# Optimization experiments

Hardware: AMD Instinct MI355X
Metric: run time of the kernel (lower is better)

The kernel has to match this reference:

```python
import jax, jax.numpy as jnp
import numpy as np

N = 8192

def _gcn_layer(x, src, dst, W, b, norm_out, norm_in, activation=None):
    # DGL GraphConv, norm='both': D_in^{-1/2} A D_out^{-1/2} X W + b
    xw = x @ W                              # [N, out] (weight first: in>=out)
    m = (xw * norm_out[:, None])[src]       # gather per-edge messages [E, out]
    agg = jax.ops.segment_sum(m, dst, num_segments=N)
    h = agg * norm_in[:, None] + b
    return activation(h) if activation is not None else h


def setup_inputs() -> dict:
    key = jax.random.key(0)
    k1, k2, k3, k4, k5 = jax.random.split(key, 5)
    E = 262144
    in_dim, h1, h2 = 512, 256, 64
    features = jax.random.normal(k1, (N, in_dim), dtype=jnp.float32)
    src = jax.random.randint(k2, (E,), 0, N)
    dst = jax.random.randint(k3, (E,), 0, N)
    W1 = jax.random.normal(k4, (in_dim, h1), dtype=jnp.float32) / np.sqrt(in_dim)
    b1 = jnp.zeros((h1,), dtype=jnp.float32)
    W2 = jax.random.normal(k5, (h1, h2), dtype=jnp.float32) / np.sqrt(h1)
    b2 = jnp.zeros((h2,), dtype=jnp.float32)
    return {"features": features, "src": src, "dst": dst,
            "W1": W1, "b1": b1, "W2": W2, "b2": b2}


def reference(features, src, dst, W1, b1, W2, b2):
    # Degrees and symmetric normalization (clamp(min=1) as in DGL GraphConv).
    ones = jnp.ones(src.shape[0], dtype=features.dtype)
    deg_out = jax.ops.segment_sum(ones, src, num_segments=N)
    deg_in = jax.ops.segment_sum(ones, dst, num_segments=N)
    norm_out = jnp.maximum(deg_out, 1.0) ** -0.5
    norm_in = jnp.maximum(deg_in, 1.0) ** -0.5
    # Encoder (dropout is identity in eval mode).
    h = _gcn_layer(features, src, dst, W1, b1, norm_out, norm_in, jax.nn.relu)
    z = _gcn_layer(h, src, dst, W2, b2, norm_out, norm_in, None)
    # Dot-product decoder.
    adj_rec = jax.nn.sigmoid(z @ z.T)       # [N, N]
    return adj_rec
```

## Files before the change

### kernel.cpp

```cpp
#include <hip/hip_runtime.h>
#include <hip/hip_bf16.h>
#include <math.h>

#define NNODES 8192
#define NEDGES 262144
#define INDIM  512
#define H1     256
#define H2     64

typedef __attribute__((ext_vector_type(8))) short bf16x8;
typedef __attribute__((ext_vector_type(4))) float f32x4;


__global__ void deg_kernel(const int* __restrict__ src, const int* __restrict__ dst,
                           int* deg_out, int* deg_in) {
    int e = blockIdx.x * blockDim.x + threadIdx.x;
    if (e < NEDGES) {
        atomicAdd(&deg_out[src[e]], 1);
        atomicAdd(&deg_in[dst[e]], 1);
    }
}

__global__ void norm_kernel(const int* __restrict__ deg_out, const int* __restrict__ deg_in,
                            float* norm_out, float* norm_in) {
    int i = blockIdx.x * blockDim.x + threadIdx.x;
    if (i < NNODES) {
        norm_out[i] = 1.0f / sqrtf(fmaxf((float)deg_out[i], 1.0f));
        norm_in[i]  = 1.0f / sqrtf(fmaxf((float)deg_in[i],  1.0f));
    }
}

__global__ __launch_bounds__(1024) void scan_kernel(const int* __restrict__ deg_in,
                                                    int* __restrict__ row_start) {
    __shared__ int part[1024];
    int t = threadIdx.x;
    int v[8]; int s = 0;
#pragma unroll
    for (int u = 0; u < 8; u++) { v[u] = deg_in[t * 8 + u]; s += v[u]; }
    part[t] = s; __syncthreads();
    for (int off = 1; off < 1024; off <<= 1) {
        int x = part[t];
        if (t >= off) x += part[t - off];
        __syncthreads();
        part[t] = x;
        __syncthreads();
    }
    int run = part[t] - s;
#pragma unroll
    for (int u = 0; u < 8; u++) { row_start[t * 8 + u] = run; run += v[u]; }
    if (t == 1023) row_start[NNODES] = run;
}

__global__ void bucket_kernel(const int* __restrict__ src, const int* __restrict__ dst,
                              const int* __restrict__ row_start,
                              int* cursor, int* __restrict__ sorted_src) {
    int e = blockIdx.x * blockDim.x + threadIdx.x;
    if (e < NEDGES) {
        int d = dst[e];
        int p = atomicAdd(&cursor[d], 1);
        sorted_src[row_start[d] + p] = src[e];
    }
}


template<int K, int NC>
__global__ __launch_bounds__(256) void gemm_scale_kernel(const float* __restrict__ X,
                                                         const float* __restrict__ W,
                                                         const float* __restrict__ scale,
                                                         float* __restrict__ out) {
    __shared__ float As[16][68];
    __shared__ float Bs[16][68];
    const int tx = threadIdx.x, ty = threadIdx.y;
    const int tid = ty * 16 + tx;
    const int i0 = blockIdx.x * 64;
    const int j0 = blockIdx.y * 64;
    float acc[4][4] = {};

    for (int k0 = 0; k0 < K; k0 += 16) {
        {
            int r = tid >> 2, kq = (tid & 3) * 4;
            float4 va = *(const float4*)&X[(size_t)(i0 + r) * K + k0 + kq];
            As[kq + 0][r] = va.x; As[kq + 1][r] = va.y;
            As[kq + 2][r] = va.z; As[kq + 3][r] = va.w;
        }
        {
            int kk = tid >> 4, cq = (tid & 15) * 4;
            float4 vb = *(const float4*)&W[(size_t)(k0 + kk) * NC + j0 + cq];
            *(float4*)&Bs[kk][cq] = vb;
        }
        __syncthreads();
#pragma unroll
        for (int kk = 0; kk < 16; kk++) {
            float4 a4 = *(float4*)&As[kk][ty * 4];
            float4 b4 = *(float4*)&Bs[kk][tx * 4];
            float av[4] = {a4.x, a4.y, a4.z, a4.w};
            float bv[4] = {b4.x, b4.y, b4.z, b4.w};
#pragma unroll
            for (int ii = 0; ii < 4; ii++)
#pragma unroll
                for (int jj = 0; jj < 4; jj++)
                    acc[ii][jj] += av[ii] * bv[jj];
        }
        __syncthreads();
    }
#pragma unroll
    for (int ii = 0; ii < 4; ii++) {
        int row = i0 + ty * 4 + ii;
        float sc = scale[row];
        float4 o = make_float4(acc[ii][0] * sc, acc[ii][1] * sc,
                               acc[ii][2] * sc, acc[ii][3] * sc);
        *(float4*)&out[(size_t)row * NC + j0 + tx * 4] = o;
    }
}


__global__ void agg256_kernel(const int* __restrict__ row_start, const int* __restrict__ sorted_src,
                              const float* __restrict__ msg, const float* __restrict__ norm_in,
                              const float* __restrict__ bias, float* __restrict__ out) {
    int n = blockIdx.x;
    int c4 = threadIdx.x * 4;
    int e0 = row_start[n], e1 = row_start[n + 1];
    float4 acc = make_float4(0.f, 0.f, 0.f, 0.f);
    for (int e = e0; e < e1; e++) {
        int s_node = sorted_src[e];
        float4 v = *(const float4*)&msg[(size_t)s_node * H1 + c4];
        acc.x += v.x; acc.y += v.y; acc.z += v.z; acc.w += v.w;
    }
    float ni = norm_in[n];
    float4 bb = *(const float4*)&bias[c4];
    float4 h = make_float4(fmaxf(acc.x * ni + bb.x, 0.f),
                           fmaxf(acc.y * ni + bb.y, 0.f),
                           fmaxf(acc.z * ni + bb.z, 0.f),
                           fmaxf(acc.w * ni + bb.w, 0.f));
    *(float4*)&out[(size_t)n * H1 + c4] = h;
}


__global__ void agg64_bf16_kernel(const int* __restrict__ row_start, const int* __restrict__ sorted_src,
                                  const float* __restrict__ msg, const float* __restrict__ norm_in,
                                  const float* __restrict__ bias, __hip_bfloat16* __restrict__ out) {
    int n = blockIdx.x;
    int c = threadIdx.x;
    int e0 = row_start[n], e1 = row_start[n + 1];
    float acc = 0.f;
    for (int e = e0; e < e1; e++) {
        int s_node = sorted_src[e];
        acc += msg[(size_t)s_node * H2 + c];
    }
    float h = acc * norm_in[n] + bias[c];
    out[(size_t)n * H2 + c] = __float2bfloat16(h);
}


__global__ __launch_bounds__(256) void decoder_mfma_kernel(const __hip_bfloat16* __restrict__ zbf,
                                                           float* __restrict__ out) {
    const short* zb = (const short*)zbf;
    const int lane = threadIdx.x & 63;
    const int wid  = threadIdx.x >> 6;
    const int i0 = blockIdx.y * 128 + wid * 32;
    const int j0 = blockIdx.x * 128;
    const int fr = lane & 15;
    const int kg = lane >> 4;

    f32x4 acc[2][8] = {};
#pragma unroll
    for (int ks = 0; ks < 2; ks++) {
        bf16x8 a[2], b[8];
#pragma unroll
        for (int m = 0; m < 2; m++)
            a[m] = *(const bf16x8*)&zb[(size_t)(i0 + m * 16 + fr) * H2 + ks * 32 + kg * 8];
#pragma unroll
        for (int n = 0; n < 8; n++)
            b[n] = *(const bf16x8*)&zb[(size_t)(j0 + n * 16 + fr) * H2 + ks * 32 + kg * 8];
#pragma unroll
        for (int m = 0; m < 2; m++)
#pragma unroll
            for (int n = 0; n < 8; n++)
                acc[m][n] = __builtin_amdgcn_mfma_f32_16x16x32_bf16(a[m], b[n], acc[m][n], 0, 0, 0);
    }

    const int col = lane & 15;
    const int rg4 = (lane >> 4) * 4;
#pragma unroll
    for (int m = 0; m < 2; m++)
#pragma unroll
        for (int n = 0; n < 8; n++) {
            size_t base = (size_t)(i0 + m * 16 + rg4) * NNODES + j0 + n * 16 + col;
#pragma unroll
            for (int r = 0; r < 4; r++)
                out[base + (size_t)r * NNODES] = 1.f / (1.f + __expf(-acc[m][n][r]));
        }
}


extern "C" void kernel_launch(void* const* d_in, const int* in_sizes, int n_in,
                              void* d_out, int out_size, void* d_ws, size_t ws_size,
                              hipStream_t stream) {
    const float* features = (const float*)d_in[0];
    const int*   src      = (const int*)d_in[1];
    const int*   dst      = (const int*)d_in[2];
    const float* W1       = (const float*)d_in[3];
    const float* b1       = (const float*)d_in[4];
    const float* W2       = (const float*)d_in[5];
    const float* b2       = (const float*)d_in[6];
    float* out = (float*)d_out;

    char* p = (char*)d_ws;
    auto alloc = [&](size_t bytes) -> void* {
        void* q = (void*)p;
        p += (bytes + 255) & ~(size_t)255;
        return q;
    };
    int*   deg_out_i  = (int*)alloc(NNODES * 4);
    int*   deg_in_i   = (int*)alloc(NNODES * 4);
    int*   cursor     = (int*)alloc(NNODES * 4);
    int*   row_start  = (int*)alloc((NNODES + 1) * 4);
    float* norm_out   = (float*)alloc(NNODES * 4);
    float* norm_in    = (float*)alloc(NNODES * 4);
    int*   sorted_src = (int*)alloc(NEDGES * 4);
    float* xw_s       = (float*)alloc((size_t)NNODES * H1 * 4);
    float* h          = (float*)alloc((size_t)NNODES * H1 * 4);
    float* hw_s       = (float*)alloc((size_t)NNODES * H2 * 4);
    __hip_bfloat16* zb = (__hip_bfloat16*)alloc((size_t)NNODES * H2 * 2);

    hipMemsetAsync(deg_out_i, 0, 3 * NNODES * 4, stream);

    deg_kernel<<<NEDGES / 256, 256, 0, stream>>>(src, dst, deg_out_i, deg_in_i);
    norm_kernel<<<NNODES / 256, 256, 0, stream>>>(deg_out_i, deg_in_i, norm_out, norm_in);
    scan_kernel<<<1, 1024, 0, stream>>>(deg_in_i, row_start);
    bucket_kernel<<<NEDGES / 256, 256, 0, stream>>>(src, dst, row_start, cursor, sorted_src);

    gemm_scale_kernel<INDIM, H1><<<dim3(128, H1 / 64), dim3(16, 16), 0, stream>>>(
        features, W1, norm_out, xw_s);
    agg256_kernel<<<NNODES, 64, 0, stream>>>(row_start, sorted_src, xw_s, norm_in, b1, h);

    gemm_scale_kernel<H1, H2><<<dim3(128, 1), dim3(16, 16), 0, stream>>>(
        h, W2, norm_out, hw_s);
    agg64_bf16_kernel<<<NNODES, 64, 0, stream>>>(row_start, sorted_src, hw_s, norm_in, b2, zb);

    decoder_mfma_kernel<<<dim3(NNODES / 128, NNODES / 128), dim3(256), 0, stream>>>(zb, out);
}
```

Baseline: 201.9 us.

## Switch GCN pipeline to bf16 MFMA GEMMs with bf16 intermediates

Replaces the fp32 shared-memory SIMT GEMMs with bf16 MFMA GEMMs, adding kernels that cast the features to bf16 and transpose the weights into bf16. Messages and hidden activations are stored as bf16 to halve gather traffic in aggregation. The 256-wide aggregation is unrolled over two edges and the 64-wide one splits edges across wave halves with a shuffle reduction. Decoder output stores become nontemporal. Precision drops to bf16 for layer-1 inputs, and the extra cast and transpose passes add memory traffic.

```diff
diff --git a/kernel.cpp b/kernel.cpp
--- a/kernel.cpp
+++ b/kernel.cpp
@@ -10,6 +10,14 @@
 
 typedef __attribute__((ext_vector_type(8))) short bf16x8;
 typedef __attribute__((ext_vector_type(4))) float f32x4;
+
+static __device__ __forceinline__ float bf2f(unsigned short u) {
+    return __uint_as_float((unsigned)u << 16);
+}
+static __device__ __forceinline__ unsigned short f2bf(float f) {
+    __hip_bfloat16 h = __float2bfloat16(f);
+    return *(unsigned short*)&h;
+}
 
 
 __global__ void deg_kernel(const int* __restrict__ src, const int* __restrict__ dst,
@@ -63,92 +71,128 @@
 }
 
 
-template<int K, int NC>
-__global__ __launch_bounds__(256) void gemm_scale_kernel(const float* __restrict__ X,
-                                                         const float* __restrict__ W,
-                                                         const float* __restrict__ scale,
-                                                         float* __restrict__ out) {
-    __shared__ float As[16][68];
-    __shared__ float Bs[16][68];
-    const int tx = threadIdx.x, ty = threadIdx.y;
-    const int tid = ty * 16 + tx;
-    const int i0 = blockIdx.x * 64;
-    const int j0 = blockIdx.y * 64;
-    float acc[4][4] = {};
-
-    for (int k0 = 0; k0 < K; k0 += 16) {
-        {
-            int r = tid >> 2, kq = (tid & 3) * 4;
-            float4 va = *(const float4*)&X[(size_t)(i0 + r) * K + k0 + kq];
-            As[kq + 0][r] = va.x; As[kq + 1][r] = va.y;
-            As[kq + 2][r] = va.z; As[kq + 3][r] = va.w;
+__global__ void cast4_kernel(const float* __restrict__ in, __hip_bfloat16* __restrict__ out) {
+    int t = blockIdx.x * blockDim.x + threadIdx.x;
+    float4 v = ((const float4*)in)[t];
+    ushort4 o;
+    o.x = f2bf(v.x); o.y = f2bf(v.y); o.z = f2bf(v.z); o.w = f2bf(v.w);
+    ((ushort4*)out)[t] = o;
+}
+
+template<int K, int N>
+__global__ void wtrans_kernel(const float* __restrict__ W, __hip_bfloat16* __restrict__ WT) {
+    int t = blockIdx.x * blockDim.x + threadIdx.x;
+    if (t < K * N) {
+        int k = t / N, c = t % N;
+        WT[(size_t)c * K + k] = __float2bfloat16(W[t]);
+    }
+}
+
+
+template<int K, int MT, int NT, int NOUT>
+__global__ __launch_bounds__(256) void gemm_mfma_kernel(const __hip_bfloat16* __restrict__ Af,
+                                                        const __hip_bfloat16* __restrict__ BTf,
+                                                        const float* __restrict__ scale,
+                                                        __hip_bfloat16* __restrict__ outf) {
+    constexpr int AM = MT / 64;
+    constexpr int BN = NT / 16;
+    const short* A  = (const short*)Af;
+    const short* BT = (const short*)BTf;
+    short* out = (short*)outf;
+    const int lane = threadIdx.x & 63;
+    const int wid  = threadIdx.x >> 6;
+    const int i0 = blockIdx.y * MT + wid * (MT / 4);
+    const int j0 = blockIdx.x * NT;
+    const int fr = lane & 15;
+    const int kg = lane >> 4;
+
+    f32x4 acc[AM][BN] = {};
+    for (int k0 = 0; k0 < K; k0 += 32) {
+        bf16x8 a[AM], b[BN];
+#pragma unroll
+        for (int m = 0; m < AM; m++)
+            a[m] = *(const bf16x8*)&A[(size_t)(i0 + m * 16 + fr) * K + k0 + kg * 8];
+#pragma unroll
+        for (int n = 0; n < BN; n++)
+            b[n] = *(const bf16x8*)&BT[(size_t)(j0 + n * 16 + fr) * K + k0 + kg * 8];
+#pragma unroll
+        for (int m = 0; m < AM; m++)
+#pragma unroll
+            for (int n = 0; n < BN; n++)
+                acc[m][n] = __builtin_amdgcn_mfma_f32_16x16x32_bf16(a[m], b[n], acc[m][n], 0, 0, 0);
+    }
+
+    const int col = lane & 15;
+    const int rg4 = (lane >> 4) * 4;
+#pragma unroll
+    for (int m = 0; m < AM; m++)
+#pragma unroll
+        for (int r = 0; r < 4; r++) {
+            int row = i0 + m * 16 + rg4 + r;
+            float sc = scale[row];
+#pragma unroll
+            for (int n = 0; n < BN; n++)
+                out[(size_t)row * NOUT + j0 + n * 16 + col] = f2bf(acc[m][n][r] * sc);
         }
-        {
-            int kk = tid >> 4, cq = (tid & 15) * 4;
-            float4 vb = *(const float4*)&W[(size_t)(k0 + kk) * NC + j0 + cq];
-            *(float4*)&Bs[kk][cq] = vb;
-        }
-        __syncthreads();
-#pragma unroll
-        for (int kk = 0; kk < 16; kk++) {
-            float4 a4 = *(float4*)&As[kk][ty * 4];
-            float4 b4 = *(float4*)&Bs[kk][tx * 4];
-            float av[4] = {a4.x, a4.y, a4.z, a4.w};
-            float bv[4] = {b4.x, b4.y, b4.z, b4.w};
-#pragma unroll
-            for (int ii = 0; ii < 4; ii++)
-#pragma unroll
-                for (int jj = 0; jj < 4; jj++)
-                    acc[ii][jj] += av[ii] * bv[jj];
-        }
-        __syncthreads();
-    }
-#pragma unroll
-    for (int ii = 0; ii < 4; ii++) {
-        int row = i0 + ty * 4 + ii;
-        float sc = scale[row];
-        float4 o = make_float4(acc[ii][0] * sc, acc[ii][1] * sc,
-                               acc[ii][2] * sc, acc[ii][3] * sc);
-        *(float4*)&out[(size_t)row * NC + j0 + tx * 4] = o;
-    }
 }
 
 
 __global__ void agg256_kernel(const int* __restrict__ row_start, const int* __restrict__ sorted_src,
-                              const float* __restrict__ msg, const float* __restrict__ norm_in,
-                              const float* __restrict__ bias, float* __restrict__ out) {
+                              const __hip_bfloat16* __restrict__ msgb, const float* __restrict__ norm_in,
+                              const float* __restrict__ bias, __hip_bfloat16* __restrict__ outb) {
+    const ushort4* msg = (const ushort4*)msgb;
     int n = blockIdx.x;
-    int c4 = threadIdx.x * 4;
+    int lane = threadIdx.x;
     int e0 = row_start[n], e1 = row_start[n + 1];
-    float4 acc = make_float4(0.f, 0.f, 0.f, 0.f);
-    for (int e = e0; e < e1; e++) {
-        int s_node = sorted_src[e];
-        float4 v = *(const float4*)&msg[(size_t)s_node * H1 + c4];
-        acc.x += v.x; acc.y += v.y; acc.z += v.z; acc.w += v.w;
+    float ax = 0.f, ay = 0.f, az = 0.f, aw = 0.f;
+    int e = e0;
+    for (; e + 1 < e1; e += 2) {
+        int s0 = sorted_src[e], s1 = sorted_src[e + 1];
+        ushort4 v0 = msg[(size_t)s0 * 64 + lane];
+        ushort4 v1 = msg[(size_t)s1 * 64 + lane];
+        ax += bf2f(v0.x) + bf2f(v1.x);
+        ay += bf2f(v0.y) + bf2f(v1.y);
+        az += bf2f(v0.z) + bf2f(v1.z);
+        aw += bf2f(v0.w) + bf2f(v1.w);
+    }
+    if (e < e1) {
+        ushort4 v0 = msg[(size_t)sorted_src[e] * 64 + lane];
+        ax += bf2f(v0.x); ay += bf2f(v0.y); az += bf2f(v0.z); aw += bf2f(v0.w);
     }
     float ni = norm_in[n];
-    float4 bb = *(const float4*)&bias[c4];
-    float4 h = make_float4(fmaxf(acc.x * ni + bb.x, 0.f),
-                           fmaxf(acc.y * ni + bb.y, 0.f),
-                           fmaxf(acc.z * ni + bb.z, 0.f),
-                           fmaxf(acc.w * ni + bb.w, 0.f));
-    *(float4*)&out[(size_t)n * H1 + c4] = h;
-}
-
-
-__global__ void agg64_bf16_kernel(const int* __restrict__ row_start, const int* __restrict__ sorted_src,
-                                  const float* __restrict__ msg, const float* __restrict__ norm_in,
-                                  const float* __restrict__ bias, __hip_bfloat16* __restrict__ out) {
+    float4 bb = ((const float4*)bias)[lane];
+    ushort4 o;
+    o.x = f2bf(fmaxf(ax * ni + bb.x, 0.f));
+    o.y = f2bf(fmaxf(ay * ni + bb.y, 0.f));
+    o.z = f2bf(fmaxf(az * ni + bb.z, 0.f));
+    o.w = f2bf(fmaxf(aw * ni + bb.w, 0.f));
+    ((ushort4*)outb)[(size_t)n * 64 + lane] = o;
+}
+
+
+__global__ void agg64_kernel(const int* __restrict__ row_start, const int* __restrict__ sorted_src,
+                             const __hip_bfloat16* __restrict__ msgb, const float* __restrict__ norm_in,
+                             const float* __restrict__ bias, __hip_bfloat16* __restrict__ outb) {
+    const unsigned* msg = (const unsigned*)msgb;
     int n = blockIdx.x;
-    int c = threadIdx.x;
+    int lane = threadIdx.x;
+    int half = lane >> 5, li = lane & 31;
     int e0 = row_start[n], e1 = row_start[n + 1];
-    float acc = 0.f;
-    for (int e = e0; e < e1; e++) {
-        int s_node = sorted_src[e];
-        acc += msg[(size_t)s_node * H2 + c];
-    }
-    float h = acc * norm_in[n] + bias[c];
-    out[(size_t)n * H2 + c] = __float2bfloat16(h);
+    float ax = 0.f, ay = 0.f;
+    for (int e = e0 + half; e < e1; e += 2) {
+        unsigned u = msg[(size_t)sorted_src[e] * 32 + li];
+        ax += bf2f((unsigned short)(u & 0xffff));
+        ay += bf2f((unsigned short)(u >> 16));
+    }
+    ax += __shfl_xor(ax, 32);
+    ay += __shfl_xor(ay, 32);
+    if (half == 0) {
+        float ni = norm_in[n];
+        float z0 = ax * ni + bias[2 * li];
+        float z1 = ay * ni + bias[2 * li + 1];
+        unsigned o = (unsigned)f2bf(z0) | ((unsigned)f2bf(z1) << 16);
+        ((unsigned*)outb)[(size_t)n * 32 + li] = o;
+    }
 }
 
 
@@ -187,8 +231,10 @@
         for (int n = 0; n < 8; n++) {
             size_t base = (size_t)(i0 + m * 16 + rg4) * NNODES + j0 + n * 16 + col;
 #pragma unroll
-            for (int r = 0; r < 4; r++)
-                out[base + (size_t)r * NNODES] = 1.f / (1.f + __expf(-acc[m][n][r]));
+            for (int r = 0; r < 4; r++) {
+                float v = 1.f / (1.f + __expf(-acc[m][n][r]));
+                __builtin_nontemporal_store(v, &out[base + (size_t)r * NNODES]);
+            }
         }
 }
 
@@ -218,10 +264,13 @@
     float* norm_out   = (float*)alloc(NNODES * 4);
     float* norm_in    = (float*)alloc(NNODES * 4);
     int*   sorted_src = (int*)alloc(NEDGES * 4);
-    float* xw_s       = (float*)alloc((size_t)NNODES * H1 * 4);
-    float* h          = (float*)alloc((size_t)NNODES * H1 * 4);
-    float* hw_s       = (float*)alloc((size_t)NNODES * H2 * 4);
-    __hip_bfloat16* zb = (__hip_bfloat16*)alloc((size_t)NNODES * H2 * 2);
+    __hip_bfloat16* featb = (__hip_bfloat16*)alloc((size_t)NNODES * INDIM * 2);
+    __hip_bfloat16* w1t   = (__hip_bfloat16*)alloc((size_t)H1 * INDIM * 2);
+    __hip_bfloat16* w2t   = (__hip_bfloat16*)alloc((size_t)H2 * H1 * 2);
+    __hip_bfloat16* xwb   = (__hip_bfloat16*)alloc((size_t)NNODES * H1 * 2);
+    __hip_bfloat16* hb    = (__hip_bfloat16*)alloc((size_t)NNODES * H1 * 2);
+    __hip_bfloat16* hwb   = (__hip_bfloat16*)alloc((size_t)NNODES * H2 * 2);
+    __hip_bfloat16* zb    = (__hip_bfloat16*)alloc((size_t)NNODES * H2 * 2);
 
     hipMemsetAsync(deg_out_i, 0, 3 * NNODES * 4, stream);
 
@@ -230,13 +279,17 @@
     scan_kernel<<<1, 1024, 0, stream>>>(deg_in_i, row_start);
     bucket_kernel<<<NEDGES / 256, 256, 0, stream>>>(src, dst, row_start, cursor, sorted_src);
 
-    gemm_scale_kernel<INDIM, H1><<<dim3(128, H1 / 64), dim3(16, 16), 0, stream>>>(
-        features, W1, norm_out, xw_s);
-    agg256_kernel<<<NNODES, 64, 0, stream>>>(row_start, sorted_src, xw_s, norm_in, b1, h);
-
-    gemm_scale_kernel<H1, H2><<<dim3(128, 1), dim3(16, 16), 0, stream>>>(
-        h, W2, norm_out, hw_s);
-    agg64_bf16_kernel<<<NNODES, 64, 0, stream>>>(row_start, sorted_src, hw_s, norm_in, b2, zb);
-
-    decoder_mfma_kernel<<<dim3(NNODES / 128, NNODES / 128), dim3(256), 0, stream>>>(zb, out);
-}
+    cast4_kernel<<<NNODES * INDIM / 4 / 256, 256, 0, stream>>>(features, featb);
+    wtrans_kernel<INDIM, H1><<<(INDIM * H1 + 255) / 256, 256, 0, stream>>>(W1, w1t);
+    wtrans_kernel<H1, H2><<<(H1 * H2 + 255) / 256, 256, 0, stream>>>(W2, w2t);
+
+    gemm_mfma_kernel<INDIM, 128, 128, H1><<<dim3(H1 / 128, NNODES / 128), 256, 0, stream>>>(
+        featb, w1t, norm_out, xwb);
+    agg256_kernel<<<NNODES, 64, 0, stream>>>(row_start, sorted_src, xwb, norm_in, b1, hb);
+
+    gemm_mfma_kernel<H1, 64, 64, H2><<<dim3(1, NNODES / 64), 256, 0, stream>>>(
+        hb, w2t, norm_out, hwb);
+    agg64_kernel<<<NNODES, 64, 0, stream>>>(row_start, sorted_src, hwb, norm_in, b2, zb);
+
+    decoder_mfma_kernel<<<dim3(NNODES / 128, NNODES / 128), 256, 0, stream>>>(zb, out);
+}
```

Result: faster. 178.7 us (-11.5%).
